# Optimization experiments

Measured on AMD Instinct MI355X. Metric: run time of the kernel, lower is better.

Reference implementation:

```python
import math
import jax, jax.numpy as jnp
import numpy as np

IN_D = 16
H_DIM = 256
NB_STEPS = 50
B = 8192


def _cc_weights(nb_steps):
    # Clenshaw-Curtis quadrature weights and nodes, exactly as the torch code.
    k = np.arange(0, nb_steps + 1, dtype=np.float64).reshape(-1, 1)
    lam = np.cos(k @ k.T * math.pi / nb_steps)
    lam[:, 0] = 0.5
    lam[:, -1] = 0.5 * lam[:, -1]
    lam = lam * 2.0 / nb_steps
    W = np.arange(0, nb_steps + 1, dtype=np.float64).reshape(-1, 1)
    W[1::2] = 0.0
    W = 2.0 / (1.0 - W ** 2)
    W[0] = 1.0
    W[1::2] = 0.0
    cc = (lam.T @ W).astype(np.float32)  # [nb_steps+1, 1]
    steps = np.cos(np.arange(0, nb_steps + 1) * math.pi / nb_steps).astype(np.float32)  # [nb_steps+1]
    return jnp.asarray(cc), jnp.asarray(steps)


def setup_inputs() -> dict:
    key = jax.random.key(0)
    ks = jax.random.split(key, 16)
    s = 0.05
    return {
        "x": jax.random.normal(ks[0], (B, 1), jnp.float32),
        "h": jax.random.normal(ks[1], (B, IN_D - 1), jnp.float32),
        "iw1": jax.random.normal(ks[2], (H_DIM, IN_D), jnp.float32) * s,
        "ib1": jax.random.normal(ks[3], (H_DIM,), jnp.float32) * s,
        "iw2": jax.random.normal(ks[4], (H_DIM, H_DIM), jnp.float32) * s,
        "ib2": jax.random.normal(ks[5], (H_DIM,), jnp.float32) * s,
        "iw3": jax.random.normal(ks[6], (1, H_DIM), jnp.float32) * s,
        "ib3": jax.random.normal(ks[7], (1,), jnp.float32) * s,
        "nw1": jax.random.normal(ks[8], (H_DIM, IN_D - 1), jnp.float32) * s,
        "nb1": jax.random.normal(ks[9], (H_DIM,), jnp.float32) * s,
        "nw2": jax.random.normal(ks[10], (H_DIM, H_DIM), jnp.float32) * s,
        "nb2": jax.random.normal(ks[11], (H_DIM,), jnp.float32) * s,
        "nw3": jax.random.normal(ks[12], (2, H_DIM), jnp.float32) * s,
        "nb3": jax.random.normal(ks[13], (2,), jnp.float32) * s,
        "nb_steps": NB_STEPS,
    }


def _integrand(z, iw1, ib1, iw2, ib2, iw3, ib3):
    # IntegrandNN: Linear-ReLU-Linear-ReLU-Linear-ELU, then +1.0
    a = jax.nn.relu(z @ iw1.T + ib1)
    a = jax.nn.relu(a @ iw2.T + ib2)
    return jax.nn.elu(a @ iw3.T + ib3) + 1.0


def reference(x, h, iw1, ib1, iw2, ib2, iw3, ib3, nw1, nb1, nw2, nb2, nw3, nb3, nb_steps):
    cc, steps = _cc_weights(int(nb_steps))  # cc: [N+1,1], steps: [N+1]
    Bn, n_pts = x.shape[0], int(nb_steps) + 1
    # x0 = 0, so quadrature nodes X_k = x * (steps_k + 1) / 2 -> [B, N+1, 1]
    X = x[:, None, :] * ((steps[None, :, None] + 1.0) * 0.5)
    Xf = X.reshape(-1, 1)                                             # [B*(N+1), 1]
    Hf = jnp.broadcast_to(h[:, None, :], (Bn, n_pts, h.shape[1])).reshape(-1, h.shape[1])
    z = jnp.concatenate([Xf, Hf], axis=1)                             # [B*(N+1), in_d]
    f = _integrand(z, iw1, ib1, iw2, ib2, iw3, ib3).reshape(Bn, n_pts, 1)
    integral = jnp.sum(f * cc[None, :, :], axis=1) * x * 0.5          # [B, 1]
    # conditioner net on h: Linear-ReLU-Linear-ReLU-Linear -> [B, 2]
    a = jax.nn.relu(h @ nw1.T + nb1)
    a = jax.nn.relu(a @ nw2.T + nb2)
    out = a @ nw3.T + nb3
    offset = out[:, :1]
    scaling = jnp.exp(out[:, 1:2])
    return scaling * integral + offset
```

## Files before the change

kernel.cpp:

```cpp
#include <hip/hip_runtime.h>
#include <hip/hip_bf16.h>
#include <math.h>

#define BATCH 8192
#define HD    256
#define NPTS  51
#define MTOT  (BATCH*NPTS)

typedef __bf16 bf16x8 __attribute__((ext_vector_type(8)));
typedef float  f32x4  __attribute__((ext_vector_type(4)));

#define OFF_IW2P  0
#define OFF_W1X   131072
#define OFF_CC    132096
#define OFF_STEPS 132352
#define OFF_OFFS  132608
#define OFF_SCAL  165376
#define OFF_G1    198144
#define OFF_FV    8586752

__device__ __forceinline__ unsigned short f2bf(float f) {
    union { float f; unsigned u; } v; v.f = f;
    unsigned r = v.u + 0x7FFFu + ((v.u >> 16) & 1u);
    return (unsigned short)(r >> 16);
}

__device__ __forceinline__ unsigned pk2bf(float lo, float hi) {
    __hip_bfloat162 t = __float22bfloat162_rn(float2{lo, hi});
    union { __hip_bfloat162 b; unsigned u; } v; v.b = t;
    return v.u;
}

__global__ void k1_fused(const float* __restrict__ iw2, const float* __restrict__ nw1,
                         const float* __restrict__ iw1, const float* __restrict__ ib1,
                         const float* __restrict__ nb1, const float* __restrict__ h,
                         const float* __restrict__ nw2, const float* __restrict__ nb2,
                         const float* __restrict__ nw3, const float* __restrict__ nb3,
                         unsigned short* iw2p, float* w1xs, float* cc, float* steps,
                         float* __restrict__ g1, float* __restrict__ offs,
                         float* __restrict__ scal) {
    int blk = blockIdx.x, tid = threadIdx.x;
    if (blk < 256) {
        int t = blk * 256 + tid;
        int n = t >> 8, k = t & 255;
        int half = n >> 7, nl = n & 127, c = k >> 3, j = k & 7;
        iw2p[half * 32768 + c * 1024 + nl * 8 + j] = f2bf(iw2[t]);
    } else if (blk == 256) {
        w1xs[tid] = iw1[tid * 16];
        const float PI_F = 3.14159265358979323846f;
        if (tid <= 50) {
            int j = tid;
            float s = 0.f;
            for (int i = 0; i <= 50; i += 2) {
                float w = (i == 0) ? 1.f : 2.f / (1.f - (float)(i * i));
                float l;
                if (j == 0 || j == 50) l = 0.5f;
                else { int r = (i * j) % 100; l = __cosf((float)r * (PI_F / 50.f)); }
                s += l * w;
            }
            cc[j]    = s * (2.f / 50.f);
            steps[j] = __cosf((float)j * (PI_F / 50.f));
        }
    } else {
        __shared__ float hs[16][15];
        __shared__ unsigned short a1s[16][264];
        __shared__ float Pp[4 * 2 * 16];
        int b0 = (blk - 257) * 16, n = tid;
        if (tid < 240) { int bb = tid / 15, j = tid % 15; hs[bb][j] = h[(b0 + bb) * 15 + j]; }
        __syncthreads();
        float ir[16], nr[15];
        const float4* ip = (const float4*)(iw1 + n * 16);
        ((float4*)ir)[0] = ip[0]; ((float4*)ir)[1] = ip[1];
        ((float4*)ir)[2] = ip[2]; ((float4*)ir)[3] = ip[3];
        #pragma unroll
        for (int j = 0; j < 15; ++j) nr[j] = nw1[n * 15 + j];
        float bi = ib1[n], bn = nb1[n];
        #pragma unroll
        for (int bb = 0; bb < 16; ++bb) {
            float g = bi, a = bn;
            #pragma unroll
            for (int j = 0; j < 15; ++j) { float hv = hs[bb][j]; g += hv * ir[j + 1]; a += hv * nr[j]; }
            g1[(b0 + bb) * 256 + n] = g;
            a1s[bb][n] = f2bf(fmaxf(a, 0.f));
        }
        __syncthreads();

        int lane = tid & 63, w = tid >> 6, l16 = lane & 15, quad = lane >> 4;
        f32x4 acc[4];
        #pragma unroll
        for (int nt = 0; nt < 4; ++nt) acc[nt] = (f32x4){0.f, 0.f, 0.f, 0.f};
        #pragma unroll
        for (int ks = 0; ks < 8; ++ks) {
            bf16x8 af = *(const bf16x8*)&a1s[l16][ks * 32 + quad * 8];
            #pragma unroll
            for (int nt = 0; nt < 4; ++nt) {
                const float* np = nw2 + (w * 64 + nt * 16 + l16) * 256 + ks * 32 + quad * 8;
                float4 f0 = ((const float4*)np)[0];
                float4 f1 = ((const float4*)np)[1];
                union { uint4 u; bf16x8 v; } bf;
                bf.u.x = pk2bf(f0.x, f0.y); bf.u.y = pk2bf(f0.z, f0.w);
                bf.u.z = pk2bf(f1.x, f1.y); bf.u.w = pk2bf(f1.z, f1.w);
                acc[nt] = __builtin_amdgcn_mfma_f32_16x16x32_bf16(af, bf.v, acc[nt], 0, 0, 0);
            }
        }
        float p0[4], p1[4];
        #pragma unroll
        for (int i = 0; i < 4; ++i) { p0[i] = 0.f; p1[i] = 0.f; }
        #pragma unroll
        for (int nt = 0; nt < 4; ++nt) {
            int nn = w * 64 + nt * 16 + l16;
            float bias = nb2[nn], wa = nw3[nn], wb = nw3[256 + nn];
            #pragma unroll
            for (int i = 0; i < 4; ++i) {
                float v = acc[nt][i] + bias;
                v = v > 0.f ? v : 0.f;
                p0[i] += v * wa;
                p1[i] += v * wb;
            }
        }
        #pragma unroll
        for (int mask = 1; mask < 16; mask <<= 1)
            #pragma unroll
            for (int i = 0; i < 4; ++i) {
                p0[i] += __shfl_xor(p0[i], mask, 64);
                p1[i] += __shfl_xor(p1[i], mask, 64);
            }
        if (l16 == 0) {
            #pragma unroll
            for (int i = 0; i < 4; ++i) {
                int r = quad * 4 + i;
                Pp[w * 32 + r]      = p0[i];
                Pp[w * 32 + 16 + r] = p1[i];
            }
        }
        __syncthreads();
        if (tid < 16) {
            float s0 = Pp[tid]      + Pp[32 + tid] + Pp[64 + tid] + Pp[96 + tid]  + nb3[0];
            float s1 = Pp[16 + tid] + Pp[48 + tid] + Pp[80 + tid] + Pp[112 + tid] + nb3[1];
            offs[b0 + tid] = s0;
            scal[b0 + tid] = __expf(s1);
        }
    }
}

__launch_bounds__(256, 2)
__global__ void k2_main(const float* __restrict__ x, const float* __restrict__ g1,
                        const float* __restrict__ w1xs, const unsigned short* __restrict__ iw2p,
                        const float* __restrict__ ib2, const float* __restrict__ iw3,
                        const float* __restrict__ steps,
                        float* __restrict__ fv) {
    __shared__ __align__(16) unsigned char smem[70656];
    float* Pp = (float*)smem;

    int tid = threadIdx.x;
    int bid = blockIdx.x;
    int m0  = bid * 128;
    int lane = tid & 63, w = tid >> 6;
    int l16 = lane & 15, quad = lane >> 4;

    unsigned blo = (unsigned)(((unsigned long long)(unsigned)m0 * 657931ull) >> 25);

    const unsigned char* bbase = (const unsigned char*)iw2p;

    #pragma unroll
    for (int hf = 0; hf < 2; ++hf)
        #pragma unroll
        for (int it = 0; it < 4; ++it)
            __builtin_amdgcn_global_load_lds(
                (const __attribute__((address_space(1))) unsigned int*)(bbase + hf * 65536 + tid * 16 + it * 4096),
                (__attribute__((address_space(3))) unsigned int*)(smem + hf * 16384 + tid * 16 + it * 4096),
                16, 0, 0);
    __builtin_amdgcn_global_load_lds(
        (const __attribute__((address_space(1))) unsigned int*)((const unsigned char*)(g1 + blo * 256) + tid * 16),
        (__attribute__((address_space(3))) unsigned int*)(smem + 65536 + tid * 16),
        16, 0, 0);
    if (w == 0)
        __builtin_amdgcn_global_load_lds(
            (const __attribute__((address_space(1))) unsigned int*)((const unsigned char*)w1xs + lane * 16),
            (__attribute__((address_space(3))) unsigned int*)(smem + 69632 + lane * 16),
            16, 0, 0);

    float xs_[2]; int rel_[2];
    #pragma unroll
    for (int mt = 0; mt < 2; ++mt) {
        int m = m0 + w * 32 + mt * 16 + l16;
        unsigned b = (unsigned)(((unsigned long long)(unsigned)m * 657931ull) >> 25);
        int p = m - (int)b * 51;
        xs_[mt] = x[b] * (steps[p] + 1.f) * 0.5f;
        rel_[mt] = (int)(b - blo) * 256;
    }

    f32x4 acc[2][16];
    #pragma unroll
    for (int mt = 0; mt < 2; ++mt)
        #pragma unroll
        for (int nt = 0; nt < 16; ++nt)
            acc[mt][nt] = (f32x4){0.f, 0.f, 0.f, 0.f};

    const float* Ag = (const float*)(smem + 65536);
    const float* Wl = (const float*)(smem + 69632);

    #pragma unroll
    for (int kc = 0; kc < 4; ++kc) {
        __syncthreads();
        if (kc < 3) {
            #pragma unroll
            for (int hf = 0; hf < 2; ++hf) {
                const unsigned char* s2 = bbase + hf * 65536 + (kc + 1) * 16384 + tid * 16;
                unsigned char* d2 = smem + ((kc + 1) & 1) * 32768 + hf * 16384 + tid * 16;
                #pragma unroll
                for (int it = 0; it < 4; ++it)
                    __builtin_amdgcn_global_load_lds(
                        (const __attribute__((address_space(1))) unsigned int*)(s2 + it * 4096),
                        (__attribute__((address_space(3))) unsigned int*)(d2 + it * 4096),
                        16, 0, 0);
            }
        }
        #pragma unroll
        for (int s = 0; s < 2; ++s) {
            int ks = kc * 2 + s;
            int ko = ks * 32 + quad * 8;
            int cl = s * 4 + quad;

            union { uint4 u; bf16x8 v; } af[2];
            {
                float4 w0 = ((const float4*)(Wl + ko))[0];
                float4 w1 = ((const float4*)(Wl + ko))[1];
                #pragma unroll
                for (int mt = 0; mt < 2; ++mt) {
                    const float* gp = Ag + rel_[mt] + ko;
                    float4 ga  = ((const float4*)gp)[0];
                    float4 gb2 = ((const float4*)gp)[1];
                    float xs = xs_[mt];
                    float a0 = fmaxf(ga.x  + xs * w0.x, 0.f);
                    float a1 = fmaxf(ga.y  + xs * w0.y, 0.f);
                    float a2 = fmaxf(ga.z  + xs * w0.z, 0.f);
                    float a3 = fmaxf(ga.w  + xs * w0.w, 0.f);
                    float a4 = fmaxf(gb2.x + xs * w1.x, 0.f);
                    float a5 = fmaxf(gb2.y + xs * w1.y, 0.f);
                    float a6 = fmaxf(gb2.z + xs * w1.z, 0.f);
                    float a7 = fmaxf(gb2.w + xs * w1.w, 0.f);
                    af[mt].u.x = pk2bf(a0, a1); af[mt].u.y = pk2bf(a2, a3);
                    af[mt].u.z = pk2bf(a4, a5); af[mt].u.w = pk2bf(a6, a7);
                }
            }

            #pragma unroll
            for (int hf = 0; hf < 2; ++hf) {
                const unsigned short* Bl = (const unsigned short*)(smem + (kc & 1) * 32768 + hf * 16384);
                #pragma unroll
                for (int g = 0; g < 2; ++g) {
                    bf16x8 bfr[4];
                    #pragma unroll
                    for (int nt = 0; nt < 4; ++nt)
                        bfr[nt] = *(const bf16x8*)(Bl + (cl * 128 + (g * 4 + nt) * 16 + l16) * 8);
                    #pragma unroll
                    for (int mt = 0; mt < 2; ++mt)
                        #pragma unroll
                        for (int nt = 0; nt < 4; ++nt)
                            acc[mt][hf * 8 + g * 4 + nt] = __builtin_amdgcn_mfma_f32_16x16x32_bf16(
                                af[mt].v, bfr[nt], acc[mt][hf * 8 + g * 4 + nt], 0, 0, 0);
                }
            }
        }
    }

    float pf[2][4];
    #pragma unroll
    for (int mt = 0; mt < 2; ++mt)
        #pragma unroll
        for (int i = 0; i < 4; ++i) pf[mt][i] = 0.f;
    #pragma unroll
    for (int idx = 0; idx < 16; ++idx) {
        int n = idx * 16 + l16;
        float bias = ib2[n], w3 = iw3[n];
        #pragma unroll
        for (int mt = 0; mt < 2; ++mt)
            #pragma unroll
            for (int i = 0; i < 4; ++i) {
                float v = acc[mt][idx][i] + bias;
                v = v > 0.f ? v : 0.f;
                pf[mt][i] += v * w3;
            }
    }
    __syncthreads();
    #pragma unroll
    for (int mt = 0; mt < 2; ++mt)
        #pragma unroll
        for (int i = 0; i < 4; ++i) {
            int row = w * 32 + mt * 16 + quad * 4 + i;
            Pp[row * 20 + l16] = pf[mt][i];
        }
    __syncthreads();
    if (tid < 128) {
        const float4* pp = (const float4*)(Pp + tid * 20);
        float4 v0 = pp[0], v1 = pp[1], v2 = pp[2], v3 = pp[3];
        float s = v0.x + v0.y + v0.z + v0.w + v1.x + v1.y + v1.z + v1.w
                + v2.x + v2.y + v2.z + v2.w + v3.x + v3.y + v3.z + v3.w;
        fv[m0 + tid] = s;
    }
}

__global__ void k4_final(const float* __restrict__ x, const float* __restrict__ fv,
                         const float* __restrict__ ib3, const float* __restrict__ cc,
                         const float* __restrict__ offs, const float* __restrict__ scal,
                         float* __restrict__ out) {
    int tid = threadIdx.x;
    int wv = tid >> 6, lane = tid & 63;
    int b = blockIdx.x * 4 + wv;
    float v = 0.f;
    if (lane < 51) {
        int m = b * 51 + lane;
        float s = fv[m] + ib3[0];
        float f = s > 0.f ? s + 1.f : __expf(s);
        v = f * cc[lane];
    }
    #pragma unroll
    for (int mask = 1; mask < 64; mask <<= 1) v += __shfl_xor(v, mask, 64);
    if (lane == 0)
        out[b] = scal[b] * (0.5f * x[b] * v) + offs[b];
}

extern "C" void kernel_launch(void* const* d_in, const int* in_sizes, int n_in,
                              void* d_out, int out_size, void* d_ws, size_t ws_size,
                              hipStream_t stream) {
    const float* x   = (const float*)d_in[0];
    const float* h   = (const float*)d_in[1];
    const float* iw1 = (const float*)d_in[2];
    const float* ib1 = (const float*)d_in[3];
    const float* iw2 = (const float*)d_in[4];
    const float* ib2 = (const float*)d_in[5];
    const float* iw3 = (const float*)d_in[6];
    const float* ib3 = (const float*)d_in[7];
    const float* nw1 = (const float*)d_in[8];
    const float* nb1 = (const float*)d_in[9];
    const float* nw2 = (const float*)d_in[10];
    const float* nb2 = (const float*)d_in[11];
    const float* nw3 = (const float*)d_in[12];
    const float* nb3 = (const float*)d_in[13];
    float* out = (float*)d_out;

    char* ws = (char*)d_ws;
    unsigned short* iw2p = (unsigned short*)(ws + OFF_IW2P);
    float* w1xs  = (float*)(ws + OFF_W1X);
    float* cc    = (float*)(ws + OFF_CC);
    float* steps = (float*)(ws + OFF_STEPS);
    float* offs  = (float*)(ws + OFF_OFFS);
    float* scal  = (float*)(ws + OFF_SCAL);
    float* g1    = (float*)(ws + OFF_G1);
    float* fv    = (float*)(ws + OFF_FV);

    k1_fused<<<dim3(769), dim3(256), 0, stream>>>(iw2, nw1, iw1, ib1, nb1, h,
                                                  nw2, nb2, nw3, nb3,
                                                  iw2p, w1xs, cc, steps, g1, offs, scal);
    k2_main<<<dim3(MTOT / 128), dim3(256), 0, stream>>>(x, g1, w1xs, iw2p, ib2, iw3,
                                                        steps, fv);
    k4_final<<<dim3(BATCH / 4), dim3(256), 0, stream>>>(x, fv, ib3, cc, offs, scal, out);
}
```

Baseline: 158.0 us.

## Make k2 persistent with the full weight matrix resident in LDS

k2_main now launches 256 blocks of 512 threads. Each block loads the whole bf16 iw2 matrix (128KB) into LDS once, then loops over 256-row tiles instead of re-streaming the weights in chunks for every 128-row tile. The per-tile g1 slice is double-buffered, with the next tile's slice prefetched asynchronously. The final row reduction now uses wave shuffles instead of an LDS round trip. The large LDS footprint limits the kernel to one block per CU, and 1632 tiles over 256 blocks leaves a tail imbalance of 7 versus 6 iterations.

```diff
diff --git a/kernel.cpp b/kernel.cpp
--- a/kernel.cpp
+++ b/kernel.cpp
@@ -6,6 +6,7 @@
 #define HD    256
 #define NPTS  51
 #define MTOT  (BATCH*NPTS)
+#define NTILES 1632
 
 typedef __bf16 bf16x8 __attribute__((ext_vector_type(8)));
 typedef float  f32x4  __attribute__((ext_vector_type(4)));
@@ -143,84 +144,76 @@
     }
 }
 
-__launch_bounds__(256, 2)
+__launch_bounds__(512, 2)
 __global__ void k2_main(const float* __restrict__ x, const float* __restrict__ g1,
                         const float* __restrict__ w1xs, const unsigned short* __restrict__ iw2p,
                         const float* __restrict__ ib2, const float* __restrict__ iw3,
                         const float* __restrict__ steps,
                         float* __restrict__ fv) {
-    __shared__ __align__(16) unsigned char smem[70656];
-    float* Pp = (float*)smem;
+    __shared__ __align__(16) unsigned char smem[148480];
 
     int tid = threadIdx.x;
-    int bid = blockIdx.x;
-    int m0  = bid * 128;
     int lane = tid & 63, w = tid >> 6;
     int l16 = lane & 15, quad = lane >> 4;
 
-    unsigned blo = (unsigned)(((unsigned long long)(unsigned)m0 * 657931ull) >> 25);
-
-    const unsigned char* bbase = (const unsigned char*)iw2p;
-
     #pragma unroll
-    for (int hf = 0; hf < 2; ++hf)
-        #pragma unroll
-        for (int it = 0; it < 4; ++it)
+    for (int it = 0; it < 16; ++it)
+        __builtin_amdgcn_global_load_lds(
+            (const __attribute__((address_space(1))) unsigned int*)((const unsigned char*)iw2p + tid * 16 + it * 8192),
+            (__attribute__((address_space(3))) unsigned int*)(smem + tid * 16 + it * 8192),
+            16, 0, 0);
+    if (tid < 64)
+        __builtin_amdgcn_global_load_lds(
+            (const __attribute__((address_space(1))) unsigned int*)((const unsigned char*)w1xs + tid * 16),
+            (__attribute__((address_space(3))) unsigned int*)(smem + 147456 + tid * 16),
+            16, 0, 0);
+    {
+        int m0 = blockIdx.x * 256;
+        unsigned blo = (unsigned)(((unsigned long long)(unsigned)m0 * 657931ull) >> 25);
+        __builtin_amdgcn_global_load_lds(
+            (const __attribute__((address_space(1))) unsigned int*)((const unsigned char*)(g1 + blo * 256) + tid * 16),
+            (__attribute__((address_space(3))) unsigned int*)(smem + 131072 + tid * 16),
+            16, 0, 0);
+    }
+    __syncthreads();
+
+    const float* Wl = (const float*)(smem + 147456);
+
+    int p = 0;
+    for (int t = blockIdx.x; t < NTILES; t += 256, p ^= 1) {
+        int m0 = t * 256;
+        unsigned blo = (unsigned)(((unsigned long long)(unsigned)m0 * 657931ull) >> 25);
+
+        if (t + 256 < NTILES) {
+            int m0n = (t + 256) * 256;
+            unsigned blon = (unsigned)(((unsigned long long)(unsigned)m0n * 657931ull) >> 25);
             __builtin_amdgcn_global_load_lds(
-                (const __attribute__((address_space(1))) unsigned int*)(bbase + hf * 65536 + tid * 16 + it * 4096),
-                (__attribute__((address_space(3))) unsigned int*)(smem + hf * 16384 + tid * 16 + it * 4096),
+                (const __attribute__((address_space(1))) unsigned int*)((const unsigned char*)(g1 + blon * 256) + tid * 16),
+                (__attribute__((address_space(3))) unsigned int*)(smem + 131072 + (p ^ 1) * 8192 + tid * 16),
                 16, 0, 0);
-    __builtin_amdgcn_global_load_lds(
-        (const __attribute__((address_space(1))) unsigned int*)((const unsigned char*)(g1 + blo * 256) + tid * 16),
-        (__attribute__((address_space(3))) unsigned int*)(smem + 65536 + tid * 16),
-        16, 0, 0);
-    if (w == 0)
-        __builtin_amdgcn_global_load_lds(
-            (const __attribute__((address_space(1))) unsigned int*)((const unsigned char*)w1xs + lane * 16),
-            (__attribute__((address_space(3))) unsigned int*)(smem + 69632 + lane * 16),
-            16, 0, 0);
-
-    float xs_[2]; int rel_[2];
-    #pragma unroll
-    for (int mt = 0; mt < 2; ++mt) {
-        int m = m0 + w * 32 + mt * 16 + l16;
-        unsigned b = (unsigned)(((unsigned long long)(unsigned)m * 657931ull) >> 25);
-        int p = m - (int)b * 51;
-        xs_[mt] = x[b] * (steps[p] + 1.f) * 0.5f;
-        rel_[mt] = (int)(b - blo) * 256;
-    }
-
-    f32x4 acc[2][16];
-    #pragma unroll
-    for (int mt = 0; mt < 2; ++mt)
-        #pragma unroll
-        for (int nt = 0; nt < 16; ++nt)
-            acc[mt][nt] = (f32x4){0.f, 0.f, 0.f, 0.f};
-
-    const float* Ag = (const float*)(smem + 65536);
-    const float* Wl = (const float*)(smem + 69632);
-
-    #pragma unroll
-    for (int kc = 0; kc < 4; ++kc) {
-        __syncthreads();
-        if (kc < 3) {
-            #pragma unroll
-            for (int hf = 0; hf < 2; ++hf) {
-                const unsigned char* s2 = bbase + hf * 65536 + (kc + 1) * 16384 + tid * 16;
-                unsigned char* d2 = smem + ((kc + 1) & 1) * 32768 + hf * 16384 + tid * 16;
-                #pragma unroll
-                for (int it = 0; it < 4; ++it)
-                    __builtin_amdgcn_global_load_lds(
-                        (const __attribute__((address_space(1))) unsigned int*)(s2 + it * 4096),
-                        (__attribute__((address_space(3))) unsigned int*)(d2 + it * 4096),
-                        16, 0, 0);
-            }
-        }
-        #pragma unroll
-        for (int s = 0; s < 2; ++s) {
-            int ks = kc * 2 + s;
+        }
+
+        float xs_[2]; int rel_[2];
+        #pragma unroll
+        for (int mt = 0; mt < 2; ++mt) {
+            int m = m0 + w * 32 + mt * 16 + l16;
+            unsigned b = (unsigned)(((unsigned long long)(unsigned)m * 657931ull) >> 25);
+            int pp = m - (int)b * 51;
+            xs_[mt] = x[b] * (steps[pp] + 1.f) * 0.5f;
+            rel_[mt] = (int)(b - blo) * 256;
+        }
+        const float* Ag = (const float*)(smem + 131072 + p * 8192);
+
+        f32x4 acc[2][16];
+        #pragma unroll
+        for (int mt = 0; mt < 2; ++mt)
+            #pragma unroll
+            for (int nt = 0; nt < 16; ++nt)
+                acc[mt][nt] = (f32x4){0.f, 0.f, 0.f, 0.f};
+
+        #pragma unroll
+        for (int ks = 0; ks < 8; ++ks) {
             int ko = ks * 32 + quad * 8;
-            int cl = s * 4 + quad;
 
             union { uint4 u; bf16x8 v; } af[2];
             {
@@ -245,59 +238,58 @@
                 }
             }
 
-            #pragma unroll
-            for (int hf = 0; hf < 2; ++hf) {
-                const unsigned short* Bl = (const unsigned short*)(smem + (kc & 1) * 32768 + hf * 16384);
-                #pragma unroll
-                for (int g = 0; g < 2; ++g) {
-                    bf16x8 bfr[4];
+            int cb = (ks * 4 + quad) * 2048 + l16 * 16;
+            #pragma unroll
+            for (int g = 0; g < 4; ++g) {
+                bf16x8 bfr[4];
+                #pragma unroll
+                for (int nt = 0; nt < 4; ++nt) {
+                    int idx = g * 4 + nt;
+                    bfr[nt] = *(const bf16x8*)(smem + (idx >> 3) * 65536 + cb + (idx & 7) * 256);
+                }
+                #pragma unroll
+                for (int mt = 0; mt < 2; ++mt)
                     #pragma unroll
                     for (int nt = 0; nt < 4; ++nt)
-                        bfr[nt] = *(const bf16x8*)(Bl + (cl * 128 + (g * 4 + nt) * 16 + l16) * 8);
-                    #pragma unroll
-                    for (int mt = 0; mt < 2; ++mt)
-                        #pragma unroll
-                        for (int nt = 0; nt < 4; ++nt)
-                            acc[mt][hf * 8 + g * 4 + nt] = __builtin_amdgcn_mfma_f32_16x16x32_bf16(
-                                af[mt].v, bfr[nt], acc[mt][hf * 8 + g * 4 + nt], 0, 0, 0);
+                        acc[mt][g * 4 + nt] = __builtin_amdgcn_mfma_f32_16x16x32_bf16(
+                            af[mt].v, bfr[nt], acc[mt][g * 4 + nt], 0, 0, 0);
+            }
+        }
+
+        float pf[2][4];
+        #pragma unroll
+        for (int mt = 0; mt < 2; ++mt)
+            #pragma unroll
+            for (int i = 0; i < 4; ++i) pf[mt][i] = 0.f;
+        #pragma unroll
+        for (int idx = 0; idx < 16; ++idx) {
+            int n = idx * 16 + l16;
+            float bias = ib2[n], w3 = iw3[n];
+            #pragma unroll
+            for (int mt = 0; mt < 2; ++mt)
+                #pragma unroll
+                for (int i = 0; i < 4; ++i) {
+                    float v = acc[mt][idx][i] + bias;
+                    v = v > 0.f ? v : 0.f;
+                    pf[mt][i] += v * w3;
                 }
-            }
-        }
-    }
-
-    float pf[2][4];
-    #pragma unroll
-    for (int mt = 0; mt < 2; ++mt)
-        #pragma unroll
-        for (int i = 0; i < 4; ++i) pf[mt][i] = 0.f;
-    #pragma unroll
-    for (int idx = 0; idx < 16; ++idx) {
-        int n = idx * 16 + l16;
-        float bias = ib2[n], w3 = iw3[n];
-        #pragma unroll
-        for (int mt = 0; mt < 2; ++mt)
-            #pragma unroll
-            for (int i = 0; i < 4; ++i) {
-                float v = acc[mt][idx][i] + bias;
-                v = v > 0.f ? v : 0.f;
-                pf[mt][i] += v * w3;
-            }
-    }
-    __syncthreads();
-    #pragma unroll
-    for (int mt = 0; mt < 2; ++mt)
-        #pragma unroll
-        for (int i = 0; i < 4; ++i) {
-            int row = w * 32 + mt * 16 + quad * 4 + i;
-            Pp[row * 20 + l16] = pf[mt][i];
-        }
-    __syncthreads();
-    if (tid < 128) {
-        const float4* pp = (const float4*)(Pp + tid * 20);
-        float4 v0 = pp[0], v1 = pp[1], v2 = pp[2], v3 = pp[3];
-        float s = v0.x + v0.y + v0.z + v0.w + v1.x + v1.y + v1.z + v1.w
-                + v2.x + v2.y + v2.z + v2.w + v3.x + v3.y + v3.z + v3.w;
-        fv[m0 + tid] = s;
+        }
+        #pragma unroll
+        for (int mask = 1; mask < 16; mask <<= 1)
+            #pragma unroll
+            for (int mt = 0; mt < 2; ++mt)
+                #pragma unroll
+                for (int i = 0; i < 4; ++i)
+                    pf[mt][i] += __shfl_xor(pf[mt][i], mask, 64);
+        if (l16 == 0) {
+            #pragma unroll
+            for (int mt = 0; mt < 2; ++mt)
+                #pragma unroll
+                for (int i = 0; i < 4; ++i)
+                    fv[m0 + w * 32 + mt * 16 + quad * 4 + i] = pf[mt][i];
+        }
+
+        __syncthreads();
     }
 }
 
@@ -353,7 +345,7 @@
     k1_fused<<<dim3(769), dim3(256), 0, stream>>>(iw2, nw1, iw1, ib1, nb1, h,
                                                   nw2, nb2, nw3, nb3,
                                                   iw2p, w1xs, cc, steps, g1, offs, scal);
-    k2_main<<<dim3(MTOT / 128), dim3(256), 0, stream>>>(x, g1, w1xs, iw2p, ib2, iw3,
-                                                        steps, fv);
+    k2_main<<<dim3(256), dim3(512), 0, stream>>>(x, g1, w1xs, iw2p, ib2, iw3,
+                                                 steps, fv);
     k4_final<<<dim3(BATCH / 4), dim3(256), 0, stream>>>(x, fv, ib3, cc, offs, scal, out);
 }
```

New measurement: 171.2 us. +8.3%, slower.
